# Kernel tuning notes

Measured on AMD Instinct MI355X. Metric: run time of the kernel, lower is better.

The kernel has to match this reference:

```python
import jax, jax.numpy as jnp
import numpy as np

SMALL_CONST = 1e-8
K = 128
N = 512 * 512  # pixels


def setup_inputs() -> dict:
    key = jax.random.key(0)
    ks = jax.random.split(key, 6)
    pos = jax.random.uniform(ks[0], (N, 2), jnp.float32, 0.0, 512.0)      # pixel coords
    mu = jax.random.uniform(ks[1], (K, 2), jnp.float32, 0.0, 512.0)       # gaussian centers
    alpha = jax.random.uniform(ks[2], (K,), jnp.float32)                   # opacities in [0,1]
    color = jax.random.uniform(ks[3], (K, 3), jnp.float32, 0.0, 255.0)     # RGB in [0,255]
    scales = 10.0 + jax.random.uniform(ks[4], (K, 2), jnp.float32) * 20.0  # anisotropic scales
    thetas = jax.random.uniform(ks[5], (K,), jnp.float32, -np.pi, np.pi)   # rotations
    return dict(pos=pos, mu=mu, alpha=alpha, color=color, scales=scales, thetas=thetas)


def _forward(pos, mu, alpha, color, scales, thetas):
    # Parameter clamps done at the top of the torch forward
    alpha = jnp.clip(alpha, 0.0, 1.0)
    color = jnp.clip(color, 0.0, 255.0)
    scales = jnp.clip(scales, 0.1, None)

    # Precompute all K inverse covariances: sigma_inv = R diag(1/s^2) R^T  -> [K,2,2]
    c, s = jnp.cos(thetas), jnp.sin(thetas)
    R = jnp.stack([jnp.stack([c, -s], -1), jnp.stack([s, c], -1)], -2)  # [K,2,2]
    inv2 = 1.0 / scales ** 2                                            # [K,2]
    sigma_inv = jnp.einsum('kti,ki,kji->ktj', R, inv2, R)               # [K,2,2]

    n = pos.shape[0]
    pc0 = jnp.zeros((n, 3), pos.dtype)
    pa0 = jnp.zeros((n, 1), pos.dtype)

    def step(carry, g):
        pc, pa = carry
        mu_k, si_k, a_k, col_k = g
        diff = pos - mu_k                                          # [N,2]
        expo = -0.5 * jnp.einsum('ni,ij,nj->n', diff, si_k, diff)  # [N]
        alpha_k = (a_k * jnp.exp(expo))[:, None]                   # [N,1]
        new_alpha = pa + alpha_k * (1.0 - pa)
        pc = (pc * pa + col_k * alpha_k * (1.0 - pa)) / (new_alpha + SMALL_CONST)
        pc = jnp.clip(pc, 0.0, 255.0)
        pa = jnp.clip(new_alpha, 0.0, 1.0)
        return (pc, pa), None

    (pc, pa), _ = jax.lax.scan(jax.checkpoint(step), (pc0, pa0),
                               (mu, sigma_inv, alpha, color))
    # include_opc=True path: append alpha channel scaled to [0,255]
    return jnp.concatenate([pc, pa * 255.0], axis=-1)  # [N,4]


def reference(pos, mu, alpha, color, scales, thetas):
    return _forward(pos, mu, alpha, color, scales, thetas)
```

## Files before the change

kernel.cpp:

```cpp
#include <hip/hip_runtime.h>
#include <math.h>

#define KG 128

typedef float f32x2 __attribute__((ext_vector_type(2)));

__global__ __launch_bounds__(128) void precompute_params(
    const float* __restrict__ mu,
    const float* __restrict__ alpha,
    const float* __restrict__ color,
    const float* __restrict__ scales,
    const float* __restrict__ thetas,
    float4* __restrict__ P0,
    float4* __restrict__ P1,
    float*  __restrict__ P2)
{
    const int k = threadIdx.x;
    if (k >= KG) return;
    const float mx = mu[2 * k];
    const float my = mu[2 * k + 1];
    const float al = fminf(fmaxf(alpha[k], 0.0f), 1.0f);
    const float cr = fminf(fmaxf(color[3 * k + 0], 0.0f), 255.0f);
    const float cg = fminf(fmaxf(color[3 * k + 1], 0.0f), 255.0f);
    const float cb = fminf(fmaxf(color[3 * k + 2], 0.0f), 255.0f);
    const float sx = fmaxf(scales[2 * k + 0], 0.1f);
    const float sy = fmaxf(scales[2 * k + 1], 0.1f);
    const float th = thetas[k];
    const float c = cosf(th);
    const float s = sinf(th);
    const float i0 = 1.0f / (sx * sx);
    const float i1 = 1.0f / (sy * sy);
    const float a  = c * c * i0 + s * s * i1;
    const float b  = c * s * (i0 - i1);
    const float cc = s * s * i0 + c * c * i1;
    const float f = -0.5f * 1.4426950408889634f;
    P0[k] = make_float4(mx, my, a * f, 2.0f * b * f);
    P1[k] = make_float4(cc * f, al, cr, cg);
    P2[k] = cb;
}

__global__ __launch_bounds__(256) void splat_fwd(
    const float* __restrict__ pos,
    const float4* __restrict__ P0,
    const float4* __restrict__ P1,
    const float*  __restrict__ P2,
    float* __restrict__ out,
    int nPairs)
{
    const int t = blockIdx.x * blockDim.x + threadIdx.x;
    if (t >= nPairs) return;

    const float4 pp = reinterpret_cast<const float4*>(pos)[t];
    const f32x2 px = { pp.x, pp.z };
    const f32x2 py = { pp.y, pp.w };

    f32x2 pa    = { 0.0f, 0.0f };
    f32x2 rprev = { 0.0f, 0.0f };
    f32x2 numr  = { 0.0f, 0.0f };
    f32x2 numg  = { 0.0f, 0.0f };
    f32x2 numb  = { 0.0f, 0.0f };

#pragma unroll 4
    for (int k = 0; k < KG; ++k) {
        const float4 q0 = P0[k];
        const float4 q1 = P1[k];
        const float  q2 = P2[k];

        const f32x2 dx = px - q0.x;
        const f32x2 dy = py - q0.y;
        const f32x2 u  = q0.z * dx + q0.w * dy;
        const f32x2 e  = dx * u + (q1.x * dy) * dy;

        f32x2 E;
        E.x = __builtin_amdgcn_exp2f(e.x);
        E.y = __builtin_amdgcn_exp2f(e.y);

        const f32x2 w   = q1.y * E;
        const f32x2 omp = 1.0f - pa;
        const f32x2 t1  = w * omp;
        const f32x2 na  = pa + t1;
        const f32x2 nae = na + 1e-8f;

        f32x2 r;
        r.x = __builtin_amdgcn_rcpf(nae.x);
        r.y = __builtin_amdgcn_rcpf(nae.y);

        const f32x2 h = rprev * pa;
        numr = numr * h + q1.z * t1;
        numg = numg * h + q1.w * t1;
        numb = numb * h + q2  * t1;

        pa.x = fminf(na.x, 1.0f);
        pa.y = fminf(na.y, 1.0f);
        rprev = r;
    }

    const f32x2 pcr = numr * rprev;
    const f32x2 pcg = numg * rprev;
    const f32x2 pcb = numb * rprev;

    float4 o0, o1;
    o0.x = fminf(fmaxf(pcr.x, 0.0f), 255.0f);
    o0.y = fminf(fmaxf(pcg.x, 0.0f), 255.0f);
    o0.z = fminf(fmaxf(pcb.x, 0.0f), 255.0f);
    o0.w = pa.x * 255.0f;
    o1.x = fminf(fmaxf(pcr.y, 0.0f), 255.0f);
    o1.y = fminf(fmaxf(pcg.y, 0.0f), 255.0f);
    o1.z = fminf(fmaxf(pcb.y, 0.0f), 255.0f);
    o1.w = pa.y * 255.0f;

    float4* o = reinterpret_cast<float4*>(out);
    o[2 * t]     = o0;
    o[2 * t + 1] = o1;
}

extern "C" void kernel_launch(void* const* d_in, const int* in_sizes, int n_in,
                              void* d_out, int out_size, void* d_ws, size_t ws_size,
                              hipStream_t stream) {
    const float* pos    = (const float*)d_in[0];
    const float* mu     = (const float*)d_in[1];
    const float* alpha  = (const float*)d_in[2];
    const float* color  = (const float*)d_in[3];
    const float* scales = (const float*)d_in[4];
    const float* thetas = (const float*)d_in[5];
    float* out = (float*)d_out;

    float4* P0 = (float4*)d_ws;
    float4* P1 = P0 + KG;
    float*  P2 = (float*)(P1 + KG);

    const int n = in_sizes[0] / 2;
    const int nPairs = n / 2;
    const int block = 256;
    const int grid = (nPairs + block - 1) / block;

    hipLaunchKernelGGL(precompute_params, dim3(1), dim3(128), 0, stream,
                       mu, alpha, color, scales, thetas, P0, P1, P2);
    hipLaunchKernelGGL(splat_fwd, dim3(grid), dim3(block), 0, stream,
                       pos, P0, P1, P2, out, nPairs);
}
```

Measured before the change: 83.70 us.

## Chunk gaussian loop into batches of eight with separated compute phases

Restructures the per-pixel compositing loop into chunks of 8 gaussians: parameters are loaded up front, the exp work is done independently per gaussian, and alpha accumulation is rewritten as a running (1-pa) product so the dependent chain is shorter. Reciprocals are computed in a separate independent phase and the per-step clamp of pa is moved to the end. This exposes more instruction-level parallelism and adds a min-waves launch bound, at the cost of higher register pressure and slightly different rounding.

```diff
diff --git a/kernel.cpp b/kernel.cpp
--- a/kernel.cpp
+++ b/kernel.cpp
@@ -2,6 +2,8 @@
 #include <math.h>
 
 #define KG 128
+#define CH 8
+#define NCHUNK (KG / CH)
 
 typedef float f32x2 __attribute__((ext_vector_type(2)));
 
@@ -39,7 +41,7 @@
     P2[k] = cb;
 }
 
-__global__ __launch_bounds__(256) void splat_fwd(
+__global__ __launch_bounds__(256, 2) void splat_fwd(
     const float* __restrict__ pos,
     const float4* __restrict__ P0,
     const float4* __restrict__ P1,
@@ -54,60 +56,79 @@
     const f32x2 px = { pp.x, pp.z };
     const f32x2 py = { pp.y, pp.w };
 
+    f32x2 omp   = { 1.0f, 1.0f };
     f32x2 pa    = { 0.0f, 0.0f };
-    f32x2 rprev = { 0.0f, 0.0f };
+    f32x2 hprev = { 0.0f, 0.0f };
+    f32x2 rlast = { 0.0f, 0.0f };
     f32x2 numr  = { 0.0f, 0.0f };
     f32x2 numg  = { 0.0f, 0.0f };
     f32x2 numb  = { 0.0f, 0.0f };
 
-#pragma unroll 4
-    for (int k = 0; k < KG; ++k) {
-        const float4 q0 = P0[k];
-        const float4 q1 = P1[k];
-        const float  q2 = P2[k];
+    for (int c = 0; c < NCHUNK; ++c) {
+        const int base = c * CH;
 
-        const f32x2 dx = px - q0.x;
-        const f32x2 dy = py - q0.y;
-        const f32x2 u  = q0.z * dx + q0.w * dy;
-        const f32x2 e  = dx * u + (q1.x * dy) * dy;
+        float4 q0[CH], q1[CH];
+        float  q2[CH];
+#pragma unroll
+        for (int j = 0; j < CH; ++j) {
+            q0[j] = P0[base + j];
+            q1[j] = P1[base + j];
+            q2[j] = P2[base + j];
+        }
 
-        f32x2 E;
-        E.x = __builtin_amdgcn_exp2f(e.x);
-        E.y = __builtin_amdgcn_exp2f(e.y);
+        f32x2 w[CH];
+#pragma unroll
+        for (int j = 0; j < CH; ++j) {
+            const f32x2 dx = px - q0[j].x;
+            const f32x2 dy = py - q0[j].y;
+            const f32x2 u  = q0[j].z * dx + q0[j].w * dy;
+            const f32x2 e  = dx * u + (q1[j].x * dy) * dy;
+            f32x2 E;
+            E.x = __builtin_amdgcn_exp2f(e.x);
+            E.y = __builtin_amdgcn_exp2f(e.y);
+            w[j] = q1[j].y * E;
+        }
 
-        const f32x2 w   = q1.y * E;
-        const f32x2 omp = 1.0f - pa;
-        const f32x2 t1  = w * omp;
-        const f32x2 na  = pa + t1;
-        const f32x2 nae = na + 1e-8f;
+        f32x2 t1[CH], paA[CH];
+#pragma unroll
+        for (int j = 0; j < CH; ++j) {
+            t1[j] = w[j] * omp;
+            omp   = omp - w[j] * omp;
+            pa    = pa + t1[j];
+            paA[j] = pa;
+        }
 
-        f32x2 r;
-        r.x = __builtin_amdgcn_rcpf(nae.x);
-        r.y = __builtin_amdgcn_rcpf(nae.y);
+        f32x2 r[CH];
+#pragma unroll
+        for (int j = 0; j < CH; ++j) {
+            const f32x2 nae = paA[j] + 1e-8f;
+            r[j].x = __builtin_amdgcn_rcpf(nae.x);
+            r[j].y = __builtin_amdgcn_rcpf(nae.y);
+        }
 
-        const f32x2 h = rprev * pa;
-        numr = numr * h + q1.z * t1;
-        numg = numg * h + q1.w * t1;
-        numb = numb * h + q2  * t1;
-
-        pa.x = fminf(na.x, 1.0f);
-        pa.y = fminf(na.y, 1.0f);
-        rprev = r;
+#pragma unroll
+        for (int j = 0; j < CH; ++j) {
+            numr = numr * hprev + q1[j].z * t1[j];
+            numg = numg * hprev + q1[j].w * t1[j];
+            numb = numb * hprev + q2[j]   * t1[j];
+            hprev = paA[j] * r[j];
+        }
+        rlast = r[CH - 1];
     }
 
-    const f32x2 pcr = numr * rprev;
-    const f32x2 pcg = numg * rprev;
-    const f32x2 pcb = numb * rprev;
+    const f32x2 pcr = numr * rlast;
+    const f32x2 pcg = numg * rlast;
+    const f32x2 pcb = numb * rlast;
 
     float4 o0, o1;
     o0.x = fminf(fmaxf(pcr.x, 0.0f), 255.0f);
     o0.y = fminf(fmaxf(pcg.x, 0.0f), 255.0f);
     o0.z = fminf(fmaxf(pcb.x, 0.0f), 255.0f);
-    o0.w = pa.x * 255.0f;
+    o0.w = fminf(pa.x, 1.0f) * 255.0f;
     o1.x = fminf(fmaxf(pcr.y, 0.0f), 255.0f);
     o1.y = fminf(fmaxf(pcg.y, 0.0f), 255.0f);
     o1.z = fminf(fmaxf(pcb.y, 0.0f), 255.0f);
-    o1.w = pa.y * 255.0f;
+    o1.w = fminf(pa.y, 1.0f) * 255.0f;
 
     float4* o = reinterpret_cast<float4*>(out);
     o[2 * t]     = o0;
```

Measured after the change: 83.44 us. About the same (-0.3%).
